# Kernel tuning notes

Hardware: AMD Instinct MI355X
Metric: run time of the kernel (lower is better)

Reference implementation:

```python
import jax, jax.numpy as jnp
import numpy as np

B, N, H, NH = 2, 1024, 1024, 16  # batch, seq per branch, hidden, heads


def setup_inputs() -> dict:
    key = jax.random.key(0)
    k1, k2, k3, k4 = jax.random.split(key, 4)
    x = jax.random.normal(k1, (B, N, H), jnp.float32)
    x2 = jax.random.normal(k2, (B, N, H), jnp.float32)
    w_qkv = jax.random.normal(k3, (3 * H, H), jnp.float32) * 0.02  # nn.Linear(H, 3H), no bias
    w_out = jax.random.normal(k4, (H, H), jnp.float32) * 0.02
    b_out = jnp.zeros((H,), jnp.float32)
    return {"x": x, "x2": x2, "w_qkv": w_qkv, "w_out": w_out, "b_out": b_out, "num_heads": NH}


def _qkv_split(x, w_qkv, nh):
    # qkv Linear then Rearrange 'b n (qkv l d) -> qkv b l n d'
    b, n, h = x.shape
    d = h // nh
    qkv = x @ w_qkv.T                                    # [b, n, 3h]
    qkv = qkv.reshape(b, n, 3, nh, d).transpose(2, 0, 3, 1, 4)  # [3, b, nh, n, d]
    return qkv[0], qkv[1], qkv[2]


def reference(x, x2, w_qkv, w_out, b_out, num_heads):
    nh = num_heads
    d = x.shape[-1] // nh
    scale = float(d) ** -0.5
    q, k, v = _qkv_split(x, w_qkv, nh)
    q2, k2, v2 = _qkv_split(x2, w_qkv, nh)
    # cross-branch concat along seq dim
    q = jnp.concatenate([q, q2], axis=2)
    k = jnp.concatenate([k, k2], axis=2)
    v = jnp.concatenate([v, v2], axis=2)
    att = jax.nn.softmax(jnp.einsum('bhxd,bhyd->bhxy', q, k) * scale, axis=-1)  # [b,nh,2N,2N]
    o = jnp.einsum('bhxy,bhyd->bhxd', att, v)            # [b,nh,2N,d]
    o1, o2 = jnp.split(o, 2, axis=2)

    def proj(o):
        b, h, n, dd = o.shape
        o = o.transpose(0, 2, 1, 3).reshape(b, n, h * dd)  # 'b h l d -> b l (h d)'
        return o @ w_out.T + b_out

    return proj(o1), proj(o2)
```

## Files before the change

### kernel.cpp

```cpp
#include <hip/hip_runtime.h>
#include <hip/hip_bf16.h>

#define NB      2
#define NSEQ    1024
#define S2      2048
#define HDIM    1024
#define NHEADS  16
#define DHEAD   64
#define Q_SCALE 0.18033688011112042f

typedef unsigned short ushort_t;
typedef __attribute__((ext_vector_type(8))) short short8;
typedef __attribute__((ext_vector_type(4))) float f32x4;
typedef __attribute__((ext_vector_type(16))) float f32x16;

__device__ __forceinline__ ushort_t f2bf(float f) {
    union { float f; unsigned int u; } c; c.f = f;
    unsigned int u = c.u;
    u += 0x7FFFu + ((u >> 16) & 1u);
    return (ushort_t)(u >> 16);
}

__device__ __forceinline__ unsigned pack_bf16x2(float a, float b) {
    union { __hip_bfloat162 h; unsigned u; } cv;
    cv.h = __float22bfloat162_rn(float2{a, b});
    return cv.u;
}

__global__ __launch_bounds__(256) void cvt_all(
    const float* __restrict__ x, const float* __restrict__ x2,
    const float* __restrict__ wqkv, const float* __restrict__ wout,
    ushort_t* __restrict__ Xb, ushort_t* __restrict__ Wqb, ushort_t* __restrict__ Wob)
{
    int b = blockIdx.x;
    const float* s; ushort_t* d; int i;
    if (b < 2048)      { s = x;    d = Xb;            i = b * 256 + threadIdx.x; }
    else if (b < 4096) { s = x2;   d = Xb + 2097152;  i = (b - 2048) * 256 + threadIdx.x; }
    else if (b < 7168) { s = wqkv; d = Wqb;           i = (b - 4096) * 256 + threadIdx.x; }
    else               { s = wout; d = Wob;           i = (b - 7168) * 256 + threadIdx.x; }
    float4 v = ((const float4*)s)[i];
    ushort4 o; o.x = f2bf(v.x); o.y = f2bf(v.y); o.z = f2bf(v.z); o.w = f2bf(v.w);
    ((ushort4*)d)[i] = o;
}

__global__ __launch_bounds__(256) void qkv_gemm_mfma(
    const ushort_t* __restrict__ Xb, const ushort_t* __restrict__ Wqb,
    ushort_t* __restrict__ Qb, ushort_t* __restrict__ Kb, ushort_t* __restrict__ Vtb)
{
    __shared__ ushort_t As[2 * 128 * 32];
    __shared__ ushort_t Bs[2 * 128 * 32];
    __shared__ float    Sc[4][16 * 20];
    const int t = threadIdx.x;
    const int lane = t & 63, quad = lane >> 4, l15 = lane & 15;
    const int w = t >> 6;
    const int wm = (w >> 1) * 64, wn = (w & 1) * 64;
    const int r0 = blockIdx.y * 128, c0 = blockIdx.x * 128;

    const int g_chunk = (lane & 3) ^ ((lane >> 3) & 3);
    const int srow_lo = w * 16 + (lane >> 2);

    auto stage = [&](int k0, int buf) {
        #pragma unroll
        for (int p = 0; p < 2; ++p) {
            int row = srow_lo + p * 64;
            const ushort_t* gpA = Xb  + (size_t)(r0 + row) * HDIM + k0 + g_chunk * 8;
            const ushort_t* gpB = Wqb + (size_t)(c0 + row) * HDIM + k0 + g_chunk * 8;
            ushort_t* lpA = As + buf * 4096 + p * 2048 + w * 512;
            ushort_t* lpB = Bs + buf * 4096 + p * 2048 + w * 512;
            __builtin_amdgcn_global_load_lds(
                (const __attribute__((address_space(1))) void*)gpA,
                (__attribute__((address_space(3))) void*)lpA, 16, 0, 0);
            __builtin_amdgcn_global_load_lds(
                (const __attribute__((address_space(1))) void*)gpB,
                (__attribute__((address_space(3))) void*)lpB, 16, 0, 0);
        }
    };

    f32x4 acc[4][4];
    #pragma unroll
    for (int i = 0; i < 4; ++i)
        #pragma unroll
        for (int j = 0; j < 4; ++j) acc[i][j] = (f32x4){0.f, 0.f, 0.f, 0.f};

    stage(0, 0);
    stage(32, 1);
    __syncthreads();

    const int sw = (l15 >> 1) & 3;
    for (int it = 0; it < 32; ++it) {
        const ushort_t* a = As + (it & 1) * 4096;
        const ushort_t* b = Bs + (it & 1) * 4096;
        short8 af[4], bf[4];
        #pragma unroll
        for (int mi = 0; mi < 4; ++mi) {
            int ra = wm + mi * 16 + l15;
            af[mi] = *(const short8*)(a + ra * 32 + ((quad ^ sw) * 8));
        }
        #pragma unroll
        for (int ni = 0; ni < 4; ++ni) {
            int rb = wn + ni * 16 + l15;
            bf[ni] = *(const short8*)(b + rb * 32 + ((quad ^ sw) * 8));
        }
        #pragma unroll
        for (int mi = 0; mi < 4; ++mi)
            #pragma unroll
            for (int ni = 0; ni < 4; ++ni)
                acc[mi][ni] = __builtin_amdgcn_mfma_f32_16x16x32_bf16(af[mi], bf[ni], acc[mi][ni], 0, 0, 0);
        __syncthreads();
        if (it < 30) stage((it + 2) * 32, it & 1);
    }

    const int branch = r0 >> 11;
    const int bb     = (r0 & 2047) >> 10;
    const int qi     = c0 >> 10;
    float* sc = &Sc[w][0];

    if (qi == 2) {
        #pragma unroll
        for (int mi = 0; mi < 4; ++mi) {
            int sbase = branch * NSEQ + (r0 & 1023) + wm + mi * 16 + quad * 4;
            #pragma unroll
            for (int ni = 0; ni < 4; ++ni) {
                int cc = (c0 & 1023) + wn + ni * 16;
                int h  = cc >> 6;
                int dd = (cc & 63) + l15;
                ushort4 pv;
                pv.x = f2bf(acc[mi][ni][0]); pv.y = f2bf(acc[mi][ni][1]);
                pv.z = f2bf(acc[mi][ni][2]); pv.w = f2bf(acc[mi][ni][3]);
                *(ushort4*)(Vtb + ((size_t)(bb * NHEADS + h) * DHEAD + dd) * S2 + sbase) = pv;
            }
        }
    } else {
        const float qsc = (qi == 0) ? Q_SCALE : 1.0f;
        ushort_t* base = (qi ? Kb : Qb);
        const int row = lane >> 2, ch = lane & 3;
        #pragma unroll
        for (int mi = 0; mi < 4; ++mi) {
            int sb = branch * NSEQ + (r0 & 1023) + wm + mi * 16;
            #pragma unroll
            for (int ni = 0; ni < 4; ++ni) {
                int cc = (c0 & 1023) + wn + ni * 16;
                int h  = cc >> 6;
                int db = cc & 63;
                #pragma unroll
                for (int reg = 0; reg < 4; ++reg)
                    sc[(quad * 4 + reg) * 20 + l15] = acc[mi][ni][reg] * qsc;
                float4 v = *(const float4*)&sc[row * 20 + ch * 4];
                uint2 pk;
                pk.x = pack_bf16x2(v.x, v.y);
                pk.y = pack_bf16x2(v.z, v.w);
                *(uint2*)(base + ((size_t)(bb * NHEADS + h) * S2 + sb + row) * DHEAD + db + ch * 4) = pk;
            }
        }
    }
}

__global__ __launch_bounds__(256) void attn_mfma(
    const ushort_t* __restrict__ Qb, const ushort_t* __restrict__ Kb,
    const ushort_t* __restrict__ Vtb, ushort_t* __restrict__ Ob)
{
    __shared__ ushort_t Ks[3 * 64 * 64];
    __shared__ ushort_t Vs[3 * 64 * 64];

    const int t = threadIdx.x, lane = t & 63, w = t >> 6;
    const int l31 = lane & 31, hi = lane >> 5;

    const int id  = blockIdx.x;
    const int j   = id >> 3;
    const int bh  = ((j & 3) << 3) | (id & 7);
    const int r0  = (j >> 2) * 128;

    const ushort_t* Qh  = Qb  + (size_t)bh * S2 * DHEAD;
    const ushort_t* Kh  = Kb  + (size_t)bh * S2 * DHEAD;
    const ushort_t* Vth = Vtb + (size_t)bh * DHEAD * S2;

    const int slot = lane & 7;
    const int rsub = lane >> 3;
    auto prefetch = [&](int kt_, int buf_) {
        #pragma unroll
        for (int c = 0; c < 2; ++c) {
            int row = w * 16 + c * 8 + rsub;
            int g   = slot ^ (row & 7);
            const ushort_t* gpK = Kh  + (size_t)(kt_ * 64 + row) * DHEAD + g * 8;
            const ushort_t* gpV = Vth + (size_t)row * S2 + kt_ * 64 + g * 8;
            ushort_t* lpK = &Ks[buf_ * 4096 + w * 1024 + c * 512];
            ushort_t* lpV = &Vs[buf_ * 4096 + w * 1024 + c * 512];
            __builtin_amdgcn_global_load_lds(
                (const __attribute__((address_space(1))) void*)gpK,
                (__attribute__((address_space(3))) void*)lpK, 16, 0, 0);
            __builtin_amdgcn_global_load_lds(
                (const __attribute__((address_space(1))) void*)gpV,
                (__attribute__((address_space(3))) void*)lpV, 16, 0, 0);
        }
    };

    short8 aq[4];
    {
        const ushort_t* qp = Qh + (size_t)(r0 + 32 * w + l31) * DHEAD + hi * 8;
        #pragma unroll
        for (int sd = 0; sd < 4; ++sd) aq[sd] = *(const short8*)(qp + sd * 16);
    }

    const int s7 = l31 & 7;
    int offA[4];
    #pragma unroll
    for (int s = 0; s < 4; ++s)
        offA[s] = (l31 * 64 + (((s * 2 + hi) ^ s7) * 8)) * 2;

    f32x16 oacc0, oacc1;
    #pragma unroll
    for (int i = 0; i < 16; ++i) { oacc0[i] = 0.f; oacc1[i] = 0.f; }
    float la0 = 0.f, la1 = 0.f, la2 = 0.f, la3 = 0.f;

    prefetch(0, 0);
    prefetch(1, 1);

    int bi = 0;
    for (int kt = 0; kt < S2 / 64; ++kt) {
        if (kt < S2 / 64 - 1) asm volatile("s_waitcnt vmcnt(4)" ::: "memory");
        else                  asm volatile("s_waitcnt vmcnt(0)" ::: "memory");
        __builtin_amdgcn_s_barrier();
        __builtin_amdgcn_sched_barrier(0);

        const char* kb = (const char*)Ks + bi * 8192;
        const char* vb = (const char*)Vs + bi * 8192;

        f32x16 s0, s1;
        #pragma unroll
        for (int i = 0; i < 16; ++i) { s0[i] = 0.f; s1[i] = 0.f; }
        __builtin_amdgcn_s_setprio(1);
        #pragma unroll
        for (int sd = 0; sd < 4; ++sd) {
            short8 k0 = *(const short8*)(kb + offA[sd]);
            short8 k1 = *(const short8*)(kb + offA[sd] + 4096);
            s0 = __builtin_amdgcn_mfma_f32_32x32x16_bf16(k0, aq[sd], s0, 0, 0, 0);
            s1 = __builtin_amdgcn_mfma_f32_32x32x16_bf16(k1, aq[sd], s1, 0, 0, 0);
        }
        __builtin_amdgcn_s_setprio(0);

        unsigned pw[4][4];
        #pragma unroll
        for (int half = 0; half < 2; ++half) {
            float p[8], q[8];
            #pragma unroll
            for (int jj = 0; jj < 8; ++jj) {
                p[jj] = __builtin_exp2f(s0[half * 8 + jj]);
                q[jj] = __builtin_exp2f(s1[half * 8 + jj]);
            }
            la0 += p[0] + p[4]; la1 += p[1] + p[5];
            la2 += p[2] + p[6]; la3 += p[3] + p[7];
            la0 += q[0] + q[4]; la1 += q[1] + q[5];
            la2 += q[2] + q[6]; la3 += q[3] + q[7];

            unsigned a0 = pack_bf16x2(p[0], p[1]), b0 = pack_bf16x2(p[2], p[3]);
            unsigned c0 = pack_bf16x2(p[4], p[5]), d0 = pack_bf16x2(p[6], p[7]);
            asm("v_permlane32_swap_b32 %0, %1" : "+v"(a0), "+v"(c0));
            asm("v_permlane32_swap_b32 %0, %1" : "+v"(b0), "+v"(d0));
            pw[half][0] = a0; pw[half][1] = b0; pw[half][2] = c0; pw[half][3] = d0;

            unsigned a1 = pack_bf16x2(q[0], q[1]), b1 = pack_bf16x2(q[2], q[3]);
            unsigned c1 = pack_bf16x2(q[4], q[5]), d1 = pack_bf16x2(q[6], q[7]);
            asm("v_permlane32_swap_b32 %0, %1" : "+v"(a1), "+v"(c1));
            asm("v_permlane32_swap_b32 %0, %1" : "+v"(b1), "+v"(d1));
            pw[2 + half][0] = a1; pw[2 + half][1] = b1; pw[2 + half][2] = c1; pw[2 + half][3] = d1;
        }

        __builtin_amdgcn_s_setprio(1);
        #pragma unroll
        for (int sk = 0; sk < 4; ++sk) {
            union { unsigned u[4]; short8 s8; } pa;
            pa.u[0] = pw[sk][0]; pa.u[1] = pw[sk][1];
            pa.u[2] = pw[sk][2]; pa.u[3] = pw[sk][3];
            short8 v0 = *(const short8*)(vb + offA[sk]);
            short8 v1 = *(const short8*)(vb + offA[sk] + 4096);
            oacc0 = __builtin_amdgcn_mfma_f32_32x32x16_bf16(pa.s8, v0, oacc0, 0, 0, 0);
            oacc1 = __builtin_amdgcn_mfma_f32_32x32x16_bf16(pa.s8, v1, oacc1, 0, 0, 0);
        }
        __builtin_amdgcn_s_setprio(0);

        if (kt + 2 < S2 / 64) {
            int pb = bi + 2; if (pb >= 3) pb -= 3;
            prefetch(kt + 2, pb);
        }
        bi = (bi == 2) ? 0 : bi + 1;
    }

    float l = (la0 + la1) + (la2 + la3);
    l += __shfl_xor(l, 32);
    const float inv = 1.0f / l;

    ushort_t* obase = Ob + (size_t)bh * S2 * DHEAD;
    #pragma unroll
    for (int r = 0; r < 16; ++r) {
        const int ql = (r & 3) + 8 * (r >> 2) + 4 * hi;
        const float iv = __shfl(inv, ql);
        const size_t rowoff = (size_t)(r0 + 32 * w + ql) * DHEAD;
        obase[rowoff + l31]      = f2bf(oacc0[r] * iv);
        obase[rowoff + 32 + l31] = f2bf(oacc1[r] * iv);
    }
}

__global__ __launch_bounds__(256) void proj_gemm_mfma(
    const ushort_t* __restrict__ Ob, const ushort_t* __restrict__ Wob,
    const float* __restrict__ Bo, float* __restrict__ Out)
{
    __shared__ ushort_t As[2 * 128 * 32];
    __shared__ ushort_t Bs[2 * 64 * 32];
    __shared__ float    Sc[4][16 * 20];
    const int t = threadIdx.x;
    const int lane = t & 63, quad = lane >> 4, l15 = lane & 15;
    const int w = t >> 6;
    const int wm = (w >> 1) * 64, wn = (w & 1) * 32;
    const int r0 = blockIdx.y * 128, c0 = blockIdx.x * 64;
    const int branch = r0 >> 11, bb = (r0 & 2047) >> 10;

    const int g_chunk = (lane & 3) ^ ((lane >> 3) & 3);
    const int srow_lo = w * 16 + (lane >> 2);

    auto stage = [&](int k0, int buf) {
        int h = k0 >> 6, off = k0 & 63;
        const ushort_t* gpB = Wob + (size_t)(c0 + srow_lo) * HDIM + k0 + g_chunk * 8;
        ushort_t* lpB = Bs + buf * 2048 + w * 512;
        __builtin_amdgcn_global_load_lds(
            (const __attribute__((address_space(1))) void*)gpB,
            (__attribute__((address_space(3))) void*)lpB, 16, 0, 0);
        #pragma unroll
        for (int p = 0; p < 2; ++p) {
            int row = srow_lo + p * 64;
            int s = branch * NSEQ + (r0 & 1023) + row;
            const ushort_t* gpA = Ob + ((size_t)(bb * NHEADS + h) * S2 + s) * DHEAD + off + g_chunk * 8;
            ushort_t* lpA = As + buf * 4096 + p * 2048 + w * 512;
            __builtin_amdgcn_global_load_lds(
                (const __attribute__((address_space(1))) void*)gpA,
                (__attribute__((address_space(3))) void*)lpA, 16, 0, 0);
        }
    };

    f32x4 acc[4][2];
    #pragma unroll
    for (int i = 0; i < 4; ++i)
        #pragma unroll
        for (int j = 0; j < 2; ++j) acc[i][j] = (f32x4){0.f, 0.f, 0.f, 0.f};

    stage(0, 0);
    stage(32, 1);
    __syncthreads();

    const int sw = (l15 >> 1) & 3;
    for (int it = 0; it < 32; ++it) {
        const ushort_t* a = As + (it & 1) * 4096;
        const ushort_t* b = Bs + (it & 1) * 2048;
        short8 af[4], bf[2];
        #pragma unroll
        for (int mi = 0; mi < 4; ++mi) {
            int ra = wm + mi * 16 + l15;
            af[mi] = *(const short8*)(a + ra * 32 + ((quad ^ sw) * 8));
        }
        #pragma unroll
        for (int ni = 0; ni < 2; ++ni) {
            int rb = wn + ni * 16 + l15;
            bf[ni] = *(const short8*)(b + rb * 32 + ((quad ^ sw) * 8));
        }
        #pragma unroll
        for (int mi = 0; mi < 4; ++mi)
            #pragma unroll
            for (int ni = 0; ni < 2; ++ni)
                acc[mi][ni] = __builtin_amdgcn_mfma_f32_16x16x32_bf16(af[mi], bf[ni], acc[mi][ni], 0, 0, 0);
        __syncthreads();
        if (it < 30) stage((it + 2) * 32, it & 1);
    }

    float* sc = &Sc[w][0];
    const int row = lane >> 2, ch = lane & 3;
    #pragma unroll
    for (int mi = 0; mi < 4; ++mi) {
        int rb0 = r0 + wm + mi * 16;
        #pragma unroll
        for (int ni = 0; ni < 2; ++ni) {
            int cb = c0 + wn + ni * 16;
            #pragma unroll
            for (int reg = 0; reg < 4; ++reg)
                sc[(quad * 4 + reg) * 20 + l15] = acc[mi][ni][reg];
            float4 v = *(const float4*)&sc[row * 20 + ch * 4];
            float4 bias = *(const float4*)&Bo[cb + ch * 4];
            v.x += bias.x; v.y += bias.y; v.z += bias.z; v.w += bias.w;
            *(float4*)&Out[(size_t)(rb0 + row) * HDIM + cb + ch * 4] = v;
        }
    }
}

extern "C" void kernel_launch(void* const* d_in, const int* in_sizes, int n_in,
                              void* d_out, int out_size, void* d_ws, size_t ws_size,
                              hipStream_t stream) {
    const float* x    = (const float*)d_in[0];
    const float* x2   = (const float*)d_in[1];
    const float* wqkv = (const float*)d_in[2];
    const float* wout = (const float*)d_in[3];
    const float* bout = (const float*)d_in[4];
    float* out = (float*)d_out;

    char* ws = (char*)d_ws;
    ushort_t* Xb  = (ushort_t*)(ws);
    ushort_t* Wqb = (ushort_t*)(ws + (8u  << 20));
    ushort_t* Wob = (ushort_t*)(ws + (14u << 20));
    ushort_t* Qb  = (ushort_t*)(ws + (16u << 20));
    ushort_t* Kb  = (ushort_t*)(ws + (24u << 20));
    ushort_t* Vtb = (ushort_t*)(ws + (32u << 20));
    ushort_t* Ob  = (ushort_t*)(ws + (40u << 20));

    cvt_all<<<8192, 256, 0, stream>>>(x, x2, wqkv, wout, Xb, Wqb, Wob);
    qkv_gemm_mfma<<<dim3(24, 32), 256, 0, stream>>>(Xb, Wqb, Qb, Kb, Vtb);
    attn_mfma<<<512, 256, 0, stream>>>(Qb, Kb, Vtb, Ob);
    proj_gemm_mfma<<<dim3(16, 32), 256, 0, stream>>>(Ob, Wob, bout, out);
}
```

Measured before the change: 209.8 us.

## Software-pipeline QK^T of next tile with softmax/PV of current tile

The attention loop is restructured so the QK^T MFMAs for tile kt+1 are issued before the exp/pack/PV work of tile kt. Two score accumulator pairs are ping-ponged, and the loop is unrolled by two. The K/V LDS ring grows from 3 to 4 buffers with a prefetch depth of 3, and the wait/barrier moves to the end of each tile. The aim is to overlap matrix-core work with the VALU-heavy softmax and to hide more global-load latency. In exchange, LDS use and register pressure rise, which may lower occupancy.

Measured after the change: 205.8 us. About the same (-1.9%).

```diff
diff --git a/kernel.cpp b/kernel.cpp
--- a/kernel.cpp
+++ b/kernel.cpp
@@ -159,8 +159,8 @@
     const ushort_t* __restrict__ Qb, const ushort_t* __restrict__ Kb,
     const ushort_t* __restrict__ Vtb, ushort_t* __restrict__ Ob)
 {
-    __shared__ ushort_t Ks[3 * 64 * 64];
-    __shared__ ushort_t Vs[3 * 64 * 64];
+    __shared__ ushort_t Ks[4 * 64 * 64];
+    __shared__ ushort_t Vs[4 * 64 * 64];
 
     const int t = threadIdx.x, lane = t & 63, w = t >> 6;
     const int l31 = lane & 31, hi = lane >> 5;
@@ -214,29 +214,31 @@
 
     prefetch(0, 0);
     prefetch(1, 1);
-
-    int bi = 0;
-    for (int kt = 0; kt < S2 / 64; ++kt) {
-        if (kt < S2 / 64 - 1) asm volatile("s_waitcnt vmcnt(4)" ::: "memory");
-        else                  asm volatile("s_waitcnt vmcnt(0)" ::: "memory");
-        __builtin_amdgcn_s_barrier();
-        __builtin_amdgcn_sched_barrier(0);
-
-        const char* kb = (const char*)Ks + bi * 8192;
-        const char* vb = (const char*)Vs + bi * 8192;
-
-        f32x16 s0, s1;
-        #pragma unroll
-        for (int i = 0; i < 16; ++i) { s0[i] = 0.f; s1[i] = 0.f; }
+    prefetch(2, 2);
+    asm volatile("s_waitcnt vmcnt(4)" ::: "memory");
+    __builtin_amdgcn_s_barrier();
+    __builtin_amdgcn_sched_barrier(0);
+
+    auto qk_tile = [&](const char* kb, f32x16& d0, f32x16& d1) {
+        #pragma unroll
+        for (int i = 0; i < 16; ++i) { d0[i] = 0.f; d1[i] = 0.f; }
         __builtin_amdgcn_s_setprio(1);
         #pragma unroll
         for (int sd = 0; sd < 4; ++sd) {
             short8 k0 = *(const short8*)(kb + offA[sd]);
             short8 k1 = *(const short8*)(kb + offA[sd] + 4096);
-            s0 = __builtin_amdgcn_mfma_f32_32x32x16_bf16(k0, aq[sd], s0, 0, 0, 0);
-            s1 = __builtin_amdgcn_mfma_f32_32x32x16_bf16(k1, aq[sd], s1, 0, 0, 0);
+            d0 = __builtin_amdgcn_mfma_f32_32x32x16_bf16(k0, aq[sd], d0, 0, 0, 0);
+            d1 = __builtin_amdgcn_mfma_f32_32x32x16_bf16(k1, aq[sd], d1, 0, 0, 0);
         }
         __builtin_amdgcn_s_setprio(0);
+    };
+
+    f32x16 sA0, sA1, sB0, sB1;
+    qk_tile((const char*)Ks, sA0, sA1);
+
+    auto tile_body = [&](f32x16& c0, f32x16& c1, f32x16& n0, f32x16& n1, int kt) {
+        if (kt < 31)
+            qk_tile((const char*)Ks + ((kt + 1) & 3) * 8192, n0, n1);
 
         unsigned pw[4][4];
         #pragma unroll
@@ -244,8 +246,8 @@
             float p[8], q[8];
             #pragma unroll
             for (int jj = 0; jj < 8; ++jj) {
-                p[jj] = __builtin_exp2f(s0[half * 8 + jj]);
-                q[jj] = __builtin_exp2f(s1[half * 8 + jj]);
+                p[jj] = __builtin_exp2f(c0[half * 8 + jj]);
+                q[jj] = __builtin_exp2f(c1[half * 8 + jj]);
             }
             la0 += p[0] + p[4]; la1 += p[1] + p[5];
             la2 += p[2] + p[6]; la3 += p[3] + p[7];
@@ -253,18 +255,19 @@
             la2 += q[2] + q[6]; la3 += q[3] + q[7];
 
             unsigned a0 = pack_bf16x2(p[0], p[1]), b0 = pack_bf16x2(p[2], p[3]);
-            unsigned c0 = pack_bf16x2(p[4], p[5]), d0 = pack_bf16x2(p[6], p[7]);
-            asm("v_permlane32_swap_b32 %0, %1" : "+v"(a0), "+v"(c0));
-            asm("v_permlane32_swap_b32 %0, %1" : "+v"(b0), "+v"(d0));
-            pw[half][0] = a0; pw[half][1] = b0; pw[half][2] = c0; pw[half][3] = d0;
+            unsigned c0_ = pack_bf16x2(p[4], p[5]), d0_ = pack_bf16x2(p[6], p[7]);
+            asm("v_permlane32_swap_b32 %0, %1" : "+v"(a0), "+v"(c0_));
+            asm("v_permlane32_swap_b32 %0, %1" : "+v"(b0), "+v"(d0_));
+            pw[half][0] = a0; pw[half][1] = b0; pw[half][2] = c0_; pw[half][3] = d0_;
 
             unsigned a1 = pack_bf16x2(q[0], q[1]), b1 = pack_bf16x2(q[2], q[3]);
-            unsigned c1 = pack_bf16x2(q[4], q[5]), d1 = pack_bf16x2(q[6], q[7]);
-            asm("v_permlane32_swap_b32 %0, %1" : "+v"(a1), "+v"(c1));
-            asm("v_permlane32_swap_b32 %0, %1" : "+v"(b1), "+v"(d1));
-            pw[2 + half][0] = a1; pw[2 + half][1] = b1; pw[2 + half][2] = c1; pw[2 + half][3] = d1;
-        }
-
+            unsigned c1_ = pack_bf16x2(q[4], q[5]), d1_ = pack_bf16x2(q[6], q[7]);
+            asm("v_permlane32_swap_b32 %0, %1" : "+v"(a1), "+v"(c1_));
+            asm("v_permlane32_swap_b32 %0, %1" : "+v"(b1), "+v"(d1_));
+            pw[2 + half][0] = a1; pw[2 + half][1] = b1; pw[2 + half][2] = c1_; pw[2 + half][3] = d1_;
+        }
+
+        const char* vb = (const char*)Vs + (kt & 3) * 8192;
         __builtin_amdgcn_s_setprio(1);
         #pragma unroll
         for (int sk = 0; sk < 4; ++sk) {
@@ -278,11 +281,22 @@
         }
         __builtin_amdgcn_s_setprio(0);
 
-        if (kt + 2 < S2 / 64) {
-            int pb = bi + 2; if (pb >= 3) pb -= 3;
-            prefetch(kt + 2, pb);
-        }
-        bi = (bi == 2) ? 0 : bi + 1;
+        if (kt <= 28) {
+            prefetch(kt + 3, (kt + 3) & 3);
+            asm volatile("s_waitcnt vmcnt(4)" ::: "memory");
+            __builtin_amdgcn_s_barrier();
+            __builtin_amdgcn_sched_barrier(0);
+        } else if (kt == 29) {
+            asm volatile("s_waitcnt vmcnt(0)" ::: "memory");
+            __builtin_amdgcn_s_barrier();
+            __builtin_amdgcn_sched_barrier(0);
+        }
+    };
+
+    #pragma unroll 1
+    for (int kt = 0; kt < 32; kt += 2) {
+        tile_body(sA0, sA1, sB0, sB1, kt);
+        tile_body(sB0, sB1, sA0, sA1, kt + 1);
     }
 
     float l = (la0 + la1) + (la2 + la3);
```
